# Optimization experiments

Hardware: AMD Instinct MI355X
Metric: run time of the kernel (lower is better)

Reference implementation:

```python
import jax, jax.numpy as jnp
import numpy as np

B, S, H = 2, 1024, 4096
NH, NKV, D = 32, 8, 128
EPS = 1e-6
THETA = 10000.0


def rotate_half(x):
    x1, x2 = jnp.split(x, 2, axis=-1)
    return jnp.concatenate([-x2, x1], axis=-1)


def rmsnorm(x, w, eps):
    # RMSNorm over the last (head_dim) axis
    var = jnp.mean(x * x, axis=-1, keepdims=True)
    return x * jax.lax.rsqrt(var + eps) * w


def setup_inputs() -> dict:
    key = jax.random.key(0)
    ks = jax.random.split(key, 6)
    hidden_states = jax.random.normal(ks[0], (B, S, H), dtype=jnp.float32)
    # scaled init so activations stay O(1)
    Wq = jax.random.normal(ks[1], (NH * D, H), dtype=jnp.float32) * (H ** -0.5)
    Wk = jax.random.normal(ks[2], (NKV * D, H), dtype=jnp.float32) * (H ** -0.5)
    Wv = jax.random.normal(ks[3], (NKV * D, H), dtype=jnp.float32) * (H ** -0.5)
    Wo = jax.random.normal(ks[4], (H, NH * D), dtype=jnp.float32) * ((NH * D) ** -0.5)
    q_norm_w = jnp.ones((D,), dtype=jnp.float32)
    k_norm_w = jnp.ones((D,), dtype=jnp.float32)
    # standard default RoPE cos/sin tables, broadcast to [B, S, D]
    pos = jnp.arange(S, dtype=jnp.float32)
    inv_freq = 1.0 / (THETA ** (jnp.arange(0, D, 2, dtype=jnp.float32) / D))
    freqs = pos[:, None] * inv_freq[None, :]            # [S, D/2]
    emb = jnp.concatenate([freqs, freqs], axis=-1)      # [S, D]
    cos = jnp.broadcast_to(jnp.cos(emb)[None], (B, S, D)).astype(jnp.float32)
    sin = jnp.broadcast_to(jnp.sin(emb)[None], (B, S, D)).astype(jnp.float32)
    return dict(hidden_states=hidden_states, cos=cos, sin=sin,
                Wq=Wq, Wk=Wk, Wv=Wv, Wo=Wo,
                q_norm_w=q_norm_w, k_norm_w=k_norm_w)


def reference(hidden_states, cos, sin, Wq, Wk, Wv, Wo, q_norm_w, k_norm_w):
    b, s, h = hidden_states.shape
    # fused QKV projections (MojoLinear: y = x @ W.T, no bias)
    q = (hidden_states @ Wq.T).reshape(b, s, NH, D)
    k = (hidden_states @ Wk.T).reshape(b, s, NKV, D)
    v = (hidden_states @ Wv.T).reshape(b, s, NKV, D)
    # per-head-dim RMSNorm on q and k, then [B, H, S, D] layout
    q = rmsnorm(q, q_norm_w, EPS).transpose(0, 2, 1, 3)   # [B, NH,  S, D]
    k = rmsnorm(k, k_norm_w, EPS).transpose(0, 2, 1, 3)   # [B, NKV, S, D]
    v = v.transpose(0, 2, 1, 3)                           # [B, NKV, S, D]
    # RoPE (rotate-half)
    c = cos[:, None, :, :]
    sn = sin[:, None, :, :]
    q = q * c + rotate_half(q) * sn
    k = k * c + rotate_half(k) * sn
    # GQA: expand KV heads to query heads
    groups = NH // NKV
    k = jnp.repeat(k, groups, axis=1)                     # [B, NH, S, D]
    v = jnp.repeat(v, groups, axis=1)
    # causal attention (prefill with empty paged cache == causal SDPA)
    scores = jnp.einsum('bhqd,bhkd->bhqk', q, k) * (D ** -0.5)
    causal = jnp.tril(jnp.ones((s, s), dtype=bool))
    scores = jnp.where(causal, scores, jnp.finfo(scores.dtype).min)
    probs = jax.nn.softmax(scores, axis=-1)
    out = jnp.einsum('bhqk,bhkd->bhqd', probs, v)         # [B, NH, S, D]
    out = out.transpose(0, 2, 1, 3).reshape(b, s, NH * D)
    return out @ Wo.T
```

## Files before the change

### kernel.cpp

```cpp
#include <hip/hip_runtime.h>


typedef float  f32x4   __attribute__((ext_vector_type(4)));
typedef float  f32x16  __attribute__((ext_vector_type(16)));
typedef __bf16 bf16x8  __attribute__((ext_vector_type(8)));
typedef unsigned short u16x8 __attribute__((ext_vector_type(8)));

__device__ __forceinline__ unsigned short f2b(float f) {
    union { float f; unsigned int u; } x;
    x.f = f;
    unsigned int u = x.u;
    unsigned int r = u + 0x7fffu + ((u >> 16) & 1u);
    return (unsigned short)(r >> 16);
}
__device__ __forceinline__ float b2f(unsigned short h) {
    union { unsigned int u; float f; } x;
    x.u = ((unsigned int)h) << 16;
    return x.f;
}

__device__ __forceinline__ void async16(const unsigned short* g, unsigned short* l) {
    __builtin_amdgcn_global_load_lds(
        (const __attribute__((address_space(1))) void*)g,
        (__attribute__((address_space(3))) void*)l, 16, 0, 0);
}

__global__ __launch_bounds__(256) void cvt(const float* __restrict__ s,
                                           unsigned short* __restrict__ d, int n8) {
    int i = blockIdx.x * 256 + threadIdx.x;
    if (i >= n8) return;
    const float4* s4 = (const float4*)s + (size_t)i * 2;
    float4 a = s4[0], b = s4[1];
    u16x8 o;
    o[0] = f2b(a.x); o[1] = f2b(a.y); o[2] = f2b(a.z); o[3] = f2b(a.w);
    o[4] = f2b(b.x); o[5] = f2b(b.y); o[6] = f2b(b.z); o[7] = f2b(b.w);
    *((u16x8*)d + i) = o;
}

template<bool BF16OUT>
__global__ __launch_bounds__(256) void gemm_bt_bf16(const unsigned short* __restrict__ A,
                                                    const unsigned short* __restrict__ W,
                                                    void* __restrict__ Cv,
                                                    int K, int N) {
    __shared__ __align__(16) unsigned short As[128 * 64];
    __shared__ __align__(16) unsigned short Bs[128 * 64];

    const int tid  = threadIdx.x;
    const int wave = tid >> 6, lane = tid & 63;
    const int wm   = wave >> 1, wn = wave & 1;
    const int l31  = lane & 31, lh = lane >> 5;
    const int arow = blockIdx.y * 128, brow = blockIdx.x * 128;

    int rr[4], gc[4], slot[4];
    #pragma unroll
    for (int it = 0; it < 4; it++) {
        slot[it] = it * 4 + wave;
        int ci = slot[it] * 64 + lane;
        rr[it] = ci >> 3;
        int c  = ci & 7;
        gc[it] = c ^ (rr[it] & 7);
    }

    f32x16 acc[2][2] = {};

    for (int k0 = 0; k0 < K; k0 += 64) {
        #pragma unroll
        for (int it = 0; it < 4; it++) {
            async16(A + (size_t)(arow + rr[it]) * K + k0 + gc[it] * 8, &As[slot[it] * 512]);
            async16(W + (size_t)(brow + rr[it]) * K + k0 + gc[it] * 8, &Bs[slot[it] * 512]);
        }
        __syncthreads();

        bf16x8 af[4][2], bfr[4][2];
        #pragma unroll
        for (int ks = 0; ks < 4; ks++) {
            #pragma unroll
            for (int i = 0; i < 2; i++) {
                int rowa = wm * 64 + i * 32 + l31;
                int ch   = (ks * 2 + lh) ^ (rowa & 7);
                af[ks][i]  = *(const bf16x8*)&As[rowa * 64 + ch * 8];
                int rowb = wn * 64 + i * 32 + l31;
                int chb  = (ks * 2 + lh) ^ (rowb & 7);
                bfr[ks][i] = *(const bf16x8*)&Bs[rowb * 64 + chb * 8];
            }
        }
        #pragma unroll
        for (int ks = 0; ks < 4; ks++)
            #pragma unroll
            for (int i = 0; i < 2; i++)
                #pragma unroll
                for (int j = 0; j < 2; j++)
                    acc[i][j] = __builtin_amdgcn_mfma_f32_32x32x16_bf16(af[ks][i], bfr[ks][j], acc[i][j], 0, 0, 0);
        __syncthreads();
    }

    #pragma unroll
    for (int i = 0; i < 2; i++)
        #pragma unroll
        for (int j = 0; j < 2; j++)
            #pragma unroll
            for (int r = 0; r < 16; r++) {
                int row = arow + wm * 64 + i * 32 + lh * 4 + (r & 3) + 8 * (r >> 2);
                int col = brow + wn * 64 + j * 32 + l31;
                if (BF16OUT)
                    ((unsigned short*)Cv)[(size_t)row * N + col] = f2b(acc[i][j][r]);
                else
                    ((float*)Cv)[(size_t)row * N + col] = acc[i][j][r];
            }
}

__global__ __launch_bounds__(256) void norm_rope(const unsigned short* __restrict__ X, int rstride,
                                                 const float* __restrict__ cosp,
                                                 const float* __restrict__ sinp,
                                                 const float* __restrict__ w,
                                                 unsigned short* __restrict__ Y, int nh) {
    const int wid  = blockIdx.x * 4 + (threadIdx.x >> 6);
    const int lane = threadIdx.x & 63;
    const int row  = wid / nh;
    const int h    = wid - row * nh;

    const unsigned short* xp = X + (size_t)row * rstride + h * 128;
    float x0 = b2f(xp[lane]), x1 = b2f(xp[lane + 64]);
    float ss = x0 * x0 + x1 * x1;
    #pragma unroll
    for (int off = 32; off; off >>= 1) ss += __shfl_xor(ss, off, 64);
    float r = rsqrtf(ss * (1.0f / 128.0f) + 1e-6f);
    float n0 = x0 * r * w[lane];
    float n1 = x1 * r * w[lane + 64];
    const float* cp = cosp + (size_t)row * 128;
    const float* sp = sinp + (size_t)row * 128;
    float y0 = n0 * cp[lane]      - n1 * sp[lane];
    float y1 = n1 * cp[lane + 64] + n0 * sp[lane + 64];
    const int b = row >> 10, s = row & 1023;
    unsigned short* yp = Y + (((size_t)(b * nh + h)) * 1024 + s) * 128;
    yp[lane]      = f2b(y0);
    yp[lane + 64] = f2b(y1);
}

__global__ __launch_bounds__(256) void v_trans(const unsigned short* __restrict__ V,
                                               unsigned short* __restrict__ Vt) {
    __shared__ unsigned short T[64][68];
    const int tid = threadIdx.x;
    const int st = blockIdx.x >> 1, dt = blockIdx.x & 1;
    const int bh = blockIdx.y, b = bh >> 3, h = bh & 7;

    const int sl = tid >> 2, c0 = (tid & 3) * 16;
    const unsigned short* src = V + (size_t)(b * 1024 + st * 64 + sl) * 6144 + h * 128 + dt * 64 + c0;
    *(u16x8*)&T[sl][c0]     = *(const u16x8*)(src);
    *(u16x8*)&T[sl][c0 + 8] = *(const u16x8*)(src + 8);
    __syncthreads();

    const int dgrp = tid >> 6, sl2 = tid & 63;
    unsigned short* dst = Vt + (size_t)bh * 131072 + st * 64 + sl2;
    #pragma unroll
    for (int jd = 0; jd < 16; jd++) {
        int dl = dgrp * 16 + jd;
        dst[(size_t)(dt * 64 + dl) * 1024] = T[sl2][dl];
    }
}

__global__ __launch_bounds__(256) void attn(const unsigned short* __restrict__ Qb,
                                            const unsigned short* __restrict__ Kb,
                                            const unsigned short* __restrict__ Vt,
                                            unsigned short* __restrict__ Ob) {
    __shared__ __align__(16) unsigned short Klds[128 * 128];
    __shared__ __align__(16) unsigned short Plds[4][16][136];

    const int tid  = threadIdx.x;
    const int w    = tid >> 6, lane = tid & 63;
    const int quad = lane >> 4, l15 = lane & 15;
    const int h = blockIdx.y, b = blockIdx.z, kvh = h >> 2;

    const unsigned short* Qp = Qb + ((size_t)(b * 32 + h))   * 131072;
    const unsigned short* Kp = Kb + ((size_t)(b * 8 + kvh))  * 131072;
    const unsigned short* Vp = Vt + ((size_t)(b * 8 + kvh))  * 131072;
    const float c2 = (float)(0.08838834764831845 * 1.4426950408889634);

    for (int half = 0; half < 2; half++) {
        const int qt = half ? (15 - (int)blockIdx.x) : (int)blockIdx.x;
        const int q0 = qt * 64;
        const int qrow = q0 + w * 16 + l15;

        bf16x8 qf[4];
        #pragma unroll
        for (int ks = 0; ks < 4; ks++)
            qf[ks] = *(const bf16x8*)(Qp + (size_t)qrow * 128 + ks * 32 + quad * 8);

        float l_i[4] = {0.0f, 0.0f, 0.0f, 0.0f};
        f32x4 o[8] = {};

        const int ntiles = (qt >> 1) + 1;
        const int nfull  = (qt * 64 + 1) >> 7;

        for (int kt = 0; kt < ntiles; kt++) {
            __syncthreads();
            #pragma unroll
            for (int it = 0; it < 8; it++) {
                int slot = it * 4 + w;
                int ci = slot * 64 + lane;
                int r = ci >> 4, c = ci & 15;
                int g = (c & 8) | ((c ^ r) & 7);
                async16(Kp + (size_t)(kt * 128 + r) * 128 + g * 8, &Klds[slot * 512]);
            }
            __syncthreads();

            f32x4 sacc[8] = {};
            #pragma unroll
            for (int ks = 0; ks < 4; ks++) {
                #pragma unroll
                for (int tn = 0; tn < 8; tn++) {
                    int row = tn * 16 + l15;
                    int ch  = ks * 4 + quad;
                    int chs = (ch & 8) | ((ch ^ row) & 7);
                    bf16x8 kf = *(const bf16x8*)&Klds[row * 128 + chs * 8];
                    sacc[tn] = __builtin_amdgcn_mfma_f32_16x16x32_bf16(qf[ks], kf, sacc[tn], 0, 0, 0);
                }
            }

            const bool masked = (kt >= nfull);
            #pragma unroll
            for (int r = 0; r < 4; r++) {
                const int qg = q0 + w * 16 + quad * 4 + r;
                #pragma unroll
                for (int tn = 0; tn < 8; tn++) {
                    float p = __builtin_amdgcn_exp2f(sacc[tn][r] * c2 - 17.0f);
                    if (masked && (kt * 128 + tn * 16 + l15 > qg)) p = 0.0f;
                    l_i[r] += p;
                    Plds[w][quad * 4 + r][tn * 16 + l15] = f2b(p);
                }
            }

            #pragma unroll
            for (int ks = 0; ks < 4; ks++) {
                bf16x8 pf = *(const bf16x8*)&Plds[w][l15][ks * 32 + quad * 8];
                #pragma unroll
                for (int td = 0; td < 8; td++) {
                    bf16x8 vf = *(const bf16x8*)(Vp + (size_t)(td * 16 + l15) * 1024 + kt * 128 + ks * 32 + quad * 8);
                    o[td] = __builtin_amdgcn_mfma_f32_16x16x32_bf16(pf, vf, o[td], 0, 0, 0);
                }
            }
        }

        #pragma unroll
        for (int r = 0; r < 4; r++) {
            float l = l_i[r];
            #pragma unroll
            for (int off = 8; off; off >>= 1) l += __shfl_xor(l, off, 16);
            float inv = 1.0f / l;
            const int qg = q0 + w * 16 + quad * 4 + r;
            unsigned short* op = Ob + ((size_t)(b * 1024 + qg)) * 4096 + h * 128;
            #pragma unroll
            for (int td = 0; td < 8; td++)
                op[td * 16 + l15] = f2b(o[td][r] * inv);
        }
    }
}

extern "C" void kernel_launch(void* const* d_in, const int* in_sizes, int n_in,
                              void* d_out, int out_size, void* d_ws, size_t ws_size,
                              hipStream_t stream) {
    const float* hid  = (const float*)d_in[0];
    const float* cosp = (const float*)d_in[1];
    const float* sinp = (const float*)d_in[2];
    const float* Wq   = (const float*)d_in[3];
    const float* Wk   = (const float*)d_in[4];
    const float* Wv   = (const float*)d_in[5];
    const float* Wo   = (const float*)d_in[6];
    const float* qw   = (const float*)d_in[7];
    const float* kw   = (const float*)d_in[8];
    float* out = (float*)d_out;

    char* ws = (char*)d_ws;
    unsigned short* QKVb = (unsigned short*)ws;
    unsigned short* Ob   = QKVb;
    size_t off = (size_t)2048 * 6144 * 2;
    unsigned short* hidb  = (unsigned short*)(ws + off); off += (size_t)2048 * 4096 * 2;
    unsigned short* Wqkvb = (unsigned short*)(ws + off); off += (size_t)6144 * 4096 * 2;
    unsigned short* Wob   = (unsigned short*)(ws + off); off += (size_t)4096 * 4096 * 2;
    unsigned short* Qb    = (unsigned short*)(ws + off); off += (size_t)2048 * 4096 * 2;
    unsigned short* Kb    = (unsigned short*)(ws + off); off += (size_t)2048 * 1024 * 2;
    unsigned short* Vt    = (unsigned short*)(ws + off);

    dim3 blk(256);
    cvt<<<4096, blk, 0, stream>>>(hid, hidb, 1048576);
    cvt<<<8192, blk, 0, stream>>>(Wq, Wqkvb, 2097152);
    cvt<<<2048, blk, 0, stream>>>(Wk, Wqkvb + (size_t)4096 * 4096, 524288);
    cvt<<<2048, blk, 0, stream>>>(Wv, Wqkvb + (size_t)5120 * 4096, 524288);
    cvt<<<8192, blk, 0, stream>>>(Wo, Wob, 2097152);
    gemm_bt_bf16<true><<<dim3(48, 16), blk, 0, stream>>>(hidb, Wqkvb, QKVb, 4096, 6144);
    norm_rope<<<16384, blk, 0, stream>>>(QKVb,        6144, cosp, sinp, qw, Qb, 32);
    norm_rope<<<4096,  blk, 0, stream>>>(QKVb + 4096, 6144, cosp, sinp, kw, Kb, 8);
    v_trans<<<dim3(32, 16), blk, 0, stream>>>(QKVb + 5120, Vt);
    attn<<<dim3(8, 32, 2), blk, 0, stream>>>(Qb, Kb, Vt, Ob);
    gemm_bt_bf16<false><<<dim3(32, 16), blk, 0, stream>>>(Ob, Wob, out, 4096, 4096);
}
```

Baseline: 523.7 us.

## Pack GEMM operands into tile-contiguous layout and merge conversion and norm launches

Replaces the five fp32-to-bf16 conversion launches with one kernel that also repacks hidden states and weights into 128x64 tile-contiguous, chunk-major blocks. The GEMMs can then load each tile with fully contiguous async copies and read LDS without XOR swizzling. The attention kernel now writes its output directly in the packed layout so it can feed the output projection. The Q and K norm/RoPE launches are merged into one. Risks include bank conflicts on the unswizzled LDS reads, scattered 2-byte stores in the attention epilogue, and the extra LDS staging pass in the converter.

```diff
diff --git a/kernel.cpp b/kernel.cpp
--- a/kernel.cpp
+++ b/kernel.cpp
@@ -25,49 +25,89 @@
         (__attribute__((address_space(3))) void*)l, 16, 0, 0);
 }
 
-__global__ __launch_bounds__(256) void cvt(const float* __restrict__ s,
-                                           unsigned short* __restrict__ d, int n8) {
-    int i = blockIdx.x * 256 + threadIdx.x;
-    if (i >= n8) return;
-    const float4* s4 = (const float4*)s + (size_t)i * 2;
-    float4 a = s4[0], b = s4[1];
-    u16x8 o;
-    o[0] = f2b(a.x); o[1] = f2b(a.y); o[2] = f2b(a.z); o[3] = f2b(a.w);
-    o[4] = f2b(b.x); o[5] = f2b(b.y); o[6] = f2b(b.z); o[7] = f2b(b.w);
-    *((u16x8*)d + i) = o;
+__global__ __launch_bounds__(256) void cvt_pack(const float* __restrict__ hid,
+                                                const float* __restrict__ Wq,
+                                                const float* __restrict__ Wk,
+                                                const float* __restrict__ Wv,
+                                                const float* __restrict__ Wo,
+                                                unsigned short* __restrict__ hidb,
+                                                unsigned short* __restrict__ Wqkvb,
+                                                unsigned short* __restrict__ Wob) {
+    __shared__ __align__(16) unsigned short L[8192];
+    const int t = threadIdx.x;
+    const int tile = blockIdx.x;
+
+    const float* src;
+    unsigned short* dst;
+    int kb;
+    if (tile < 1024) {
+        int rb = tile >> 6; kb = tile & 63;
+        src = hid + (size_t)rb * 128 * 4096;
+        dst = hidb + (size_t)tile * 8192;
+    } else if (tile < 4096) {
+        int tt = tile - 1024;
+        int rb = tt >> 6; kb = tt & 63;
+        dst = Wqkvb + (size_t)tt * 8192;
+        if (rb < 32)      src = Wq + (size_t)rb * 128 * 4096;
+        else if (rb < 40) src = Wk + (size_t)(rb - 32) * 128 * 4096;
+        else              src = Wv + (size_t)(rb - 40) * 128 * 4096;
+    } else {
+        int tt = tile - 4096;
+        int rb = tt >> 6; kb = tt & 63;
+        src = Wo + (size_t)rb * 128 * 4096;
+        dst = Wob + (size_t)tt * 8192;
+    }
+
+    const int r0 = t >> 2, cq = t & 3;
+    #pragma unroll
+    for (int rr = 0; rr < 2; rr++) {
+        int row = r0 + rr * 64;
+        const float* sp = src + (size_t)row * 4096 + kb * 64 + cq * 16;
+        float4 v0 = ((const float4*)sp)[0];
+        float4 v1 = ((const float4*)sp)[1];
+        float4 v2 = ((const float4*)sp)[2];
+        float4 v3 = ((const float4*)sp)[3];
+        u16x8 a, b;
+        a[0]=f2b(v0.x); a[1]=f2b(v0.y); a[2]=f2b(v0.z); a[3]=f2b(v0.w);
+        a[4]=f2b(v1.x); a[5]=f2b(v1.y); a[6]=f2b(v1.z); a[7]=f2b(v1.w);
+        b[0]=f2b(v2.x); b[1]=f2b(v2.y); b[2]=f2b(v2.z); b[3]=f2b(v2.w);
+        b[4]=f2b(v3.x); b[5]=f2b(v3.y); b[6]=f2b(v3.z); b[7]=f2b(v3.w);
+        *(u16x8*)&L[((cq * 2)     * 128 + row) * 8] = a;
+        *(u16x8*)&L[((cq * 2 + 1) * 128 + row) * 8] = b;
+    }
+    __syncthreads();
+    #pragma unroll
+    for (int j = 0; j < 4; j++)
+        *(u16x8*)(dst + t * 32 + j * 8) = *(const u16x8*)&L[t * 32 + j * 8];
 }
 
 template<bool BF16OUT>
-__global__ __launch_bounds__(256) void gemm_bt_bf16(const unsigned short* __restrict__ A,
-                                                    const unsigned short* __restrict__ W,
-                                                    void* __restrict__ Cv,
-                                                    int K, int N) {
-    __shared__ __align__(16) unsigned short As[128 * 64];
-    __shared__ __align__(16) unsigned short Bs[128 * 64];
+__global__ __launch_bounds__(256) void gemm_packed(const unsigned short* __restrict__ A,
+                                                   const unsigned short* __restrict__ W,
+                                                   void* __restrict__ Cv,
+                                                   int K, int N) {
+    __shared__ __align__(16) unsigned short As[8192];
+    __shared__ __align__(16) unsigned short Bs[8192];
 
     const int tid  = threadIdx.x;
     const int wave = tid >> 6, lane = tid & 63;
     const int wm   = wave >> 1, wn = wave & 1;
     const int l31  = lane & 31, lh = lane >> 5;
-    const int arow = blockIdx.y * 128, brow = blockIdx.x * 128;
-
-    int rr[4], gc[4], slot[4];
-    #pragma unroll
-    for (int it = 0; it < 4; it++) {
-        slot[it] = it * 4 + wave;
-        int ci = slot[it] * 64 + lane;
-        rr[it] = ci >> 3;
-        int c  = ci & 7;
-        gc[it] = c ^ (rr[it] & 7);
-    }
+    const int KT   = K >> 6;
+
+    const unsigned short* Ap = A + (size_t)blockIdx.y * KT * 8192;
+    const unsigned short* Wp = W + (size_t)blockIdx.x * KT * 8192;
 
     f32x16 acc[2][2] = {};
 
-    for (int k0 = 0; k0 < K; k0 += 64) {
+    for (int kt = 0; kt < KT; kt++) {
+        const unsigned short* at = Ap + (size_t)kt * 8192;
+        const unsigned short* wt = Wp + (size_t)kt * 8192;
         #pragma unroll
         for (int it = 0; it < 4; it++) {
-            async16(A + (size_t)(arow + rr[it]) * K + k0 + gc[it] * 8, &As[slot[it] * 512]);
-            async16(W + (size_t)(brow + rr[it]) * K + k0 + gc[it] * 8, &Bs[slot[it] * 512]);
+            int slot = it * 4 + wave;
+            async16(at + slot * 512 + lane * 8, &As[slot * 512]);
+            async16(wt + slot * 512 + lane * 8, &Bs[slot * 512]);
         }
         __syncthreads();
 
@@ -76,12 +116,9 @@
         for (int ks = 0; ks < 4; ks++) {
             #pragma unroll
             for (int i = 0; i < 2; i++) {
-                int rowa = wm * 64 + i * 32 + l31;
-                int ch   = (ks * 2 + lh) ^ (rowa & 7);
-                af[ks][i]  = *(const bf16x8*)&As[rowa * 64 + ch * 8];
-                int rowb = wn * 64 + i * 32 + l31;
-                int chb  = (ks * 2 + lh) ^ (rowb & 7);
-                bfr[ks][i] = *(const bf16x8*)&Bs[rowb * 64 + chb * 8];
+                int ch = ks * 2 + lh;
+                af[ks][i]  = *(const bf16x8*)&As[(ch * 128 + wm * 64 + i * 32 + l31) * 8];
+                bfr[ks][i] = *(const bf16x8*)&Bs[(ch * 128 + wn * 64 + i * 32 + l31) * 8];
             }
         }
         #pragma unroll
@@ -94,6 +131,7 @@
         __syncthreads();
     }
 
+    const int arow = blockIdx.y * 128, brow = blockIdx.x * 128;
     #pragma unroll
     for (int i = 0; i < 2; i++)
         #pragma unroll
@@ -109,17 +147,35 @@
             }
 }
 
-__global__ __launch_bounds__(256) void norm_rope(const unsigned short* __restrict__ X, int rstride,
-                                                 const float* __restrict__ cosp,
-                                                 const float* __restrict__ sinp,
-                                                 const float* __restrict__ w,
-                                                 unsigned short* __restrict__ Y, int nh) {
+__global__ __launch_bounds__(256) void norm_rope_qk(const unsigned short* __restrict__ X,
+                                                    const float* __restrict__ cosp,
+                                                    const float* __restrict__ sinp,
+                                                    const float* __restrict__ qw,
+                                                    const float* __restrict__ kw,
+                                                    unsigned short* __restrict__ Qb,
+                                                    unsigned short* __restrict__ Kb) {
     const int wid  = blockIdx.x * 4 + (threadIdx.x >> 6);
     const int lane = threadIdx.x & 63;
-    const int row  = wid / nh;
-    const int h    = wid - row * nh;
-
-    const unsigned short* xp = X + (size_t)row * rstride + h * 128;
+
+    const unsigned short* xp;
+    const float* w;
+    unsigned short* yp;
+    int row;
+    if (wid < 65536) {
+        row = wid >> 5;
+        int h = wid & 31;
+        xp = X + (size_t)row * 6144 + h * 128;
+        w  = qw;
+        yp = Qb + (((size_t)((row >> 10) * 32 + h)) * 1024 + (row & 1023)) * 128;
+    } else {
+        int wid2 = wid - 65536;
+        row = wid2 >> 3;
+        int h = wid2 & 7;
+        xp = X + (size_t)row * 6144 + 4096 + h * 128;
+        w  = kw;
+        yp = Kb + (((size_t)((row >> 10) * 8 + h)) * 1024 + (row & 1023)) * 128;
+    }
+
     float x0 = b2f(xp[lane]), x1 = b2f(xp[lane + 64]);
     float ss = x0 * x0 + x1 * x1;
     #pragma unroll
@@ -131,8 +187,6 @@
     const float* sp = sinp + (size_t)row * 128;
     float y0 = n0 * cp[lane]      - n1 * sp[lane];
     float y1 = n1 * cp[lane + 64] + n0 * sp[lane + 64];
-    const int b = row >> 10, s = row & 1023;
-    unsigned short* yp = Y + (((size_t)(b * nh + h)) * 1024 + s) * 128;
     yp[lane]      = f2b(y0);
     yp[lane + 64] = f2b(y1);
 }
@@ -248,10 +302,14 @@
             for (int off = 8; off; off >>= 1) l += __shfl_xor(l, off, 16);
             float inv = 1.0f / l;
             const int qg = q0 + w * 16 + quad * 4 + r;
-            unsigned short* op = Ob + ((size_t)(b * 1024 + qg)) * 4096 + h * 128;
-            #pragma unroll
-            for (int td = 0; td < 8; td++)
-                op[td * 16 + l15] = f2b(o[td][r] * inv);
+            const int rowg = b * 1024 + qg;
+            const int rb = rowg >> 7, rloc = rowg & 127;
+            #pragma unroll
+            for (int td = 0; td < 8; td++) {
+                int colg = h * 128 + td * 16 + l15;
+                size_t cell = ((size_t)(rb * 64 + (colg >> 6)) * 1024 + ((colg >> 3) & 7) * 128 + rloc);
+                Ob[cell * 8 + (colg & 7)] = f2b(o[td][r] * inv);
+            }
         }
     }
 }
@@ -282,15 +340,10 @@
     unsigned short* Vt    = (unsigned short*)(ws + off);
 
     dim3 blk(256);
-    cvt<<<4096, blk, 0, stream>>>(hid, hidb, 1048576);
-    cvt<<<8192, blk, 0, stream>>>(Wq, Wqkvb, 2097152);
-    cvt<<<2048, blk, 0, stream>>>(Wk, Wqkvb + (size_t)4096 * 4096, 524288);
-    cvt<<<2048, blk, 0, stream>>>(Wv, Wqkvb + (size_t)5120 * 4096, 524288);
-    cvt<<<8192, blk, 0, stream>>>(Wo, Wob, 2097152);
-    gemm_bt_bf16<true><<<dim3(48, 16), blk, 0, stream>>>(hidb, Wqkvb, QKVb, 4096, 6144);
-    norm_rope<<<16384, blk, 0, stream>>>(QKVb,        6144, cosp, sinp, qw, Qb, 32);
-    norm_rope<<<4096,  blk, 0, stream>>>(QKVb + 4096, 6144, cosp, sinp, kw, Kb, 8);
+    cvt_pack<<<6144, blk, 0, stream>>>(hid, Wq, Wk, Wv, Wo, hidb, Wqkvb, Wob);
+    gemm_packed<true><<<dim3(48, 16), blk, 0, stream>>>(hidb, Wqkvb, QKVb, 4096, 6144);
+    norm_rope_qk<<<20480, blk, 0, stream>>>(QKVb, cosp, sinp, qw, kw, Qb, Kb);
     v_trans<<<dim3(32, 16), blk, 0, stream>>>(QKVb + 5120, Vt);
     attn<<<dim3(8, 32, 2), blk, 0, stream>>>(Qb, Kb, Vt, Ob);
-    gemm_bt_bf16<false><<<dim3(32, 16), blk, 0, stream>>>(Ob, Wob, out, 4096, 4096);
-}
+    gemm_packed<false><<<dim3(32, 16), blk, 0, stream>>>(Ob, Wob, out, 4096, 4096);
+}
```

Result: no change. 527.6 us (+0.8%).
